# Optimization experiments

Measured on AMD Instinct MI355X. Metric: run time of the kernel, lower is better.

Reference implementation:

```python
import jax, jax.numpy as jnp
import numpy as np

OVERALL_W = (0.4, 0.4, 0.1, 0.1)


def nn_distance(pc1, pc2):
    # pc1: (B,N,3), pc2: (B,M,3) -> squared NN distance each way.
    # ||a-b||^2 = ||a||^2 + ||b||^2 - 2 a.b ; compute via batched GEMM.
    n1 = jnp.sum(pc1 * pc1, axis=-1)  # (B,N)
    n2 = jnp.sum(pc2 * pc2, axis=-1)  # (B,M)
    cross = jnp.einsum('bnd,bmd->bnm', pc1, pc2)  # (B,N,M)
    d = n1[:, :, None] + n2[:, None, :] - 2.0 * cross  # (B,N,M)
    dist1 = jnp.min(d, axis=2)  # (B,N)
    dist2 = jnp.min(d, axis=1)  # (B,M)
    return dist1, dist2


def setup_inputs() -> dict:
    key = jax.random.key(0)
    ks = jax.random.split(key, 7)
    bs, n_pts, num_hypo, cap_len = 16, 4096, 64, 77
    return {
        'shape_query': jax.random.normal(ks[0], (bs, n_pts, 3), dtype=jnp.float32),
        'logits': jax.random.normal(ks[1], (bs, num_hypo), dtype=jnp.float32),
        'pair_caption': jax.random.randint(ks[2], (bs, 2, cap_len), 0, 30000),
        'caption_embed': jax.random.randint(ks[3], (bs, 3, cap_len), 0, 30000),
        'sdf_pred': jax.random.normal(ks[4], (bs, 1, n_pts), dtype=jnp.float32),
        'prior': jax.random.normal(ks[5], (bs, 1024, 3), dtype=jnp.float32),
        'model': jax.random.normal(ks[6], (bs, 4096, 3), dtype=jnp.float32),
    }


def reference(shape_query, logits, pair_caption, caption_embed, sdf_pred, prior, model):
    log_prob = jax.nn.log_softmax(logits, axis=-1)
    pose_loss = -jnp.mean(log_prob[:, 0])
    reconstructed = jnp.concatenate([shape_query, prior], axis=1)  # (B, N+1024, 3)
    dist1, dist2 = nn_distance(reconstructed, model)
    shape_loss = jnp.mean(dist1) + jnp.mean(dist2)
    sdf_loss = shape_loss
    caption_loss = shape_loss
    loss = (OVERALL_W[0] * pose_loss + OVERALL_W[1] * shape_loss
            + OVERALL_W[2] * sdf_loss + OVERALL_W[3] * caption_loss)
    return (loss, pose_loss, shape_loss, sdf_loss, caption_loss)
```

## Files before the change

kernel.cpp:

```cpp
#include <hip/hip_runtime.h>
#include <math.h>

#define BATCH   16
#define NQ      4096
#define NPRIOR  1024
#define NREC    5120
#define NMODEL  4096
#define NHYP    64

#define NQD1    (BATCH*NREC)
#define NQD2    (BATCH*NMODEL)

#define TILE_COLS 512
#define P1_ROWBLKS (NREC/128)
#define P2_ROWBLKS (NMODEL/128)
#define P1_CHUNKS 2
#define P2_CHUNKS 2
#define P1_NTILES (NMODEL/TILE_COLS/P1_CHUNKS)
#define P2_NTILES (NREC/TILE_COLS/P2_CHUNKS)
#define P1_BLOCKS (BATCH*P1_ROWBLKS*P1_CHUNKS)
#define P2_BLOCKS (BATCH*P2_ROWBLKS*P2_CHUNKS)
#define GBLOCKS   (P1_BLOCKS + P2_BLOCKS)

#define WS_WORDS (P1_CHUNKS*NQD1 + P2_CHUNKS*NQD2 + 1)
#define WS_BYTES ((size_t)WS_WORDS*4)
#define RED_BLOCKS 128

typedef _Float16 half8  __attribute__((ext_vector_type(8)));
typedef float    f32x16 __attribute__((ext_vector_type(16)));

__device__ __forceinline__ float min3f(float a, float b, float c) {
    float d;
    asm("v_min3_f32 %0, %1, %2, %3" : "=v"(d) : "v"(a), "v"(b), "v"(c));
    return d;
}

__device__ __forceinline__ void packQ2(float x, float y, float z,
                                       half8& hi, half8& lo) {
    float n = fmaf(z, z, fmaf(y, y, x * x));
    float mx = -2.0f * x, my = -2.0f * y, mz = -2.0f * z;
    _Float16 xh = (_Float16)mx, yh = (_Float16)my, zh = (_Float16)mz;
    _Float16 nh = (_Float16)n;
    _Float16 xl = (_Float16)(mx - (float)xh);
    _Float16 yl = (_Float16)(my - (float)yh);
    _Float16 zl = (_Float16)(mz - (float)zh);
    _Float16 nl = (_Float16)(n - (float)nh);
    hi[0] = xh; hi[1] = yh; hi[2] = zh; hi[3] = nh;
    hi[4] = (_Float16)1.0f; hi[5] = xh; hi[6] = yh; hi[7] = zh;
    lo[0] = xl; lo[1] = yl; lo[2] = zl; lo[3] = nl;
    lo[4] = (_Float16)1.0f; lo[5] = (_Float16)0.0f;
    lo[6] = (_Float16)0.0f; lo[7] = (_Float16)0.0f;
}
__device__ __forceinline__ void packR2(float x, float y, float z,
                                       half8& hi, half8& lo) {
    float n = fmaf(z, z, fmaf(y, y, x * x));
    _Float16 xh = (_Float16)x, yh = (_Float16)y, zh = (_Float16)z;
    _Float16 nh = (_Float16)n;
    _Float16 xl = (_Float16)(x - (float)xh);
    _Float16 yl = (_Float16)(y - (float)yh);
    _Float16 zl = (_Float16)(z - (float)zh);
    _Float16 nl = (_Float16)(n - (float)nh);
    hi[0] = xh; hi[1] = yh; hi[2] = zh; hi[3] = (_Float16)1.0f;
    hi[4] = nh; hi[5] = xl; hi[6] = yl; hi[7] = zl;
    lo[0] = xh; lo[1] = yh; lo[2] = zh; lo[3] = (_Float16)1.0f;
    lo[4] = nl; lo[5] = (_Float16)0.0f;
    lo[6] = (_Float16)0.0f; lo[7] = (_Float16)0.0f;
}

__device__ __forceinline__ const float* rec_ptr(
    const float* __restrict__ shape_query, const float* __restrict__ prior,
    int b, int g) {
    return (g < NQ) ? shape_query + ((size_t)b * NQ + g) * 3
                    : prior + ((size_t)b * NPRIOR + (g - NQ)) * 3;
}

__global__ __launch_bounds__(256) void chamfer_hp(
    const float* __restrict__ shape_query,
    const float* __restrict__ prior,
    const float* __restrict__ model,
    float* __restrict__ ws, float* __restrict__ out) {
    __shared__ half8 Alds2[2 * 128];
    __shared__ half8 Blds2[2 * TILE_COLS];

    const int blk = blockIdx.x;
    if (blk == 0 && threadIdx.x == 0) {
        out[2] = 0.0f; out[3] = 0.0f;
        ((unsigned*)ws)[WS_WORDS - 1] = 0u;
    }

    const int t    = threadIdx.x;
    const int wave = t >> 6;
    const int lane = t & 63;
    const int l31  = lane & 31;
    const int kh   = lane >> 5;

    int b, rowbase, colbase0, ntiles;
    float* rowplane;
    const bool pass1 = (blk < P1_BLOCKS);
    if (pass1) {
        b = blk / (P1_ROWBLKS * P1_CHUNKS);
        int rem = blk % (P1_ROWBLKS * P1_CHUNKS);
        int rb = rem / P1_CHUNKS, ck = rem % P1_CHUNKS;
        rowbase = rb * 128;
        colbase0 = ck * (P1_NTILES * TILE_COLS);
        ntiles = P1_NTILES;
        rowplane = ws + (size_t)ck * NQD1 + b * NREC + rowbase;
    } else {
        int j = blk - P1_BLOCKS;
        b = j / (P2_ROWBLKS * P2_CHUNKS);
        int rem = j % (P2_ROWBLKS * P2_CHUNKS);
        int rb = rem / P2_CHUNKS, ck = rem % P2_CHUNKS;
        rowbase = rb * 128;
        colbase0 = ck * (P2_NTILES * TILE_COLS);
        ntiles = P2_NTILES;
        rowplane = ws + (size_t)P1_CHUNKS * NQD1 + (size_t)ck * NQD2
                   + b * NMODEL + rowbase;
    }

    if (t < 128) {
        const float* p = pass1
            ? rec_ptr(shape_query, prior, b, rowbase + t)
            : model + ((size_t)b * NMODEL + rowbase + t) * 3;
        half8 hi, lo;
        packQ2(p[0], p[1], p[2], hi, lo);
        Alds2[t] = hi; Alds2[128 + t] = lo;
    }

    {
        const float* p0 = pass1
            ? model + ((size_t)b * NMODEL + colbase0 + t) * 3
            : rec_ptr(shape_query, prior, b, colbase0 + t);
        const float* p1 = pass1
            ? model + ((size_t)b * NMODEL + colbase0 + 256 + t) * 3
            : rec_ptr(shape_query, prior, b, colbase0 + 256 + t);
        half8 hi, lo;
        packR2(p0[0], p0[1], p0[2], hi, lo);
        Blds2[t] = hi; Blds2[TILE_COLS + t] = lo;
        packR2(p1[0], p1[1], p1[2], hi, lo);
        Blds2[256 + t] = hi; Blds2[TILE_COLS + 256 + t] = lo;
    }

    float rmn[16];
#pragma unroll
    for (int r = 0; r < 16; ++r) rmn[r] = 3.0e38f;

    f32x16 cz;
#pragma unroll
    for (int i = 0; i < 16; ++i) cz[i] = 0.0f;

    const int boff = kh * TILE_COLS;

    __syncthreads();

    for (int tile = 0; tile < ntiles; ++tile) {
        float nx0, ny0, nz0, nx1, ny1, nz1;
        const bool more = (tile + 1 < ntiles);
        if (more) {
            const int cb = colbase0 + (tile + 1) * TILE_COLS;
            const float* p0 = pass1
                ? model + ((size_t)b * NMODEL + cb + t) * 3
                : rec_ptr(shape_query, prior, b, cb + t);
            const float* p1 = pass1
                ? model + ((size_t)b * NMODEL + cb + 256 + t) * 3
                : rec_ptr(shape_query, prior, b, cb + 256 + t);
            nx0 = p0[0]; ny0 = p0[1]; nz0 = p0[2];
            nx1 = p1[0]; ny1 = p1[1]; nz1 = p1[2];
        }

        half8 af = Alds2[kh * 128 + wave * 32 + l31];
        half8 bfa = Blds2[boff + l31];
        half8 bfb = Blds2[boff + 32 + l31];
#pragma unroll 2
        for (int it = 0; it < TILE_COLS / 64; ++it) {
            const int nxt = (it == TILE_COLS / 64 - 1) ? 0 : (it + 1) * 64;
            half8 bfa_n = Blds2[boff + nxt + l31];
            half8 bfb_n = Blds2[boff + nxt + 32 + l31];
            f32x16 da = __builtin_amdgcn_mfma_f32_32x32x16_f16(af, bfa, cz, 0, 0, 0);
            f32x16 db = __builtin_amdgcn_mfma_f32_32x32x16_f16(af, bfb, cz, 0, 0, 0);
#pragma unroll
            for (int r = 0; r < 16; ++r) rmn[r] = min3f(rmn[r], da[r], db[r]);
            bfa = bfa_n; bfb = bfb_n;
        }

        __syncthreads();
        if (more) {
            half8 hi, lo;
            packR2(nx0, ny0, nz0, hi, lo);
            Blds2[t] = hi; Blds2[TILE_COLS + t] = lo;
            packR2(nx1, ny1, nz1, hi, lo);
            Blds2[256 + t] = hi; Blds2[TILE_COLS + 256 + t] = lo;
            __syncthreads();
        }
    }

#pragma unroll
    for (int r = 0; r < 16; ++r) {
        float v = rmn[r];
        v = fminf(v, __shfl_xor(v, 1, 64));
        v = fminf(v, __shfl_xor(v, 2, 64));
        v = fminf(v, __shfl_xor(v, 4, 64));
        v = fminf(v, __shfl_xor(v, 8, 64));
        v = fminf(v, __shfl_xor(v, 16, 64));
        if (l31 == 0) {
            int row = wave * 32 + (r & 3) + 8 * (r >> 2) + 4 * kh;
            rowplane[row] = v;
        }
    }
}

__global__ __launch_bounds__(256) void reduce_finalize2(
    const float* __restrict__ ws, const float* __restrict__ logits,
    float* __restrict__ out, unsigned int* __restrict__ counter) {
    const float* p1 = ws;
    const float* p2 = ws + (size_t)P1_CHUNKS * NQD1;
    float s1 = 0.0f, s2 = 0.0f;
    const int tot = NQD1 + NQD2;
    for (int i = blockIdx.x * 256 + threadIdx.x; i < tot;
         i += RED_BLOCKS * 256) {
        if (i < NQD1) {
            s1 += fminf(p1[i], p1[NQD1 + i]);
        } else {
            int j = i - NQD1;
            s2 += fminf(p2[j], p2[NQD2 + j]);
        }
    }
#pragma unroll
    for (int off = 32; off > 0; off >>= 1) {
        s1 += __shfl_xor(s1, off, 64);
        s2 += __shfl_xor(s2, off, 64);
    }
    __shared__ float a1[4], a2[4];
    __shared__ int last;
    int w = threadIdx.x >> 6;
    if ((threadIdx.x & 63) == 0) { a1[w] = s1; a2[w] = s2; }
    __syncthreads();
    if (threadIdx.x == 0) {
        atomicAdd(&out[2], a1[0] + a1[1] + a1[2] + a1[3]);
        atomicAdd(&out[3], a2[0] + a2[1] + a2[2] + a2[3]);
        __threadfence();
        unsigned done = atomicAdd(counter, 1u);
        last = (done == RED_BLOCKS - 1) ? 1 : 0;
    }
    __syncthreads();
    if (last && threadIdx.x < 64) {
        const int lane = threadIdx.x;
        float pose_part = 0.0f;
        if (lane < BATCH) {
            const float* L = logits + lane * NHYP;
            float mx = L[0];
#pragma unroll 8
            for (int j = 1; j < NHYP; ++j) mx = fmaxf(mx, L[j]);
            float s = 0.0f;
#pragma unroll 8
            for (int j = 0; j < NHYP; ++j) s += expf(L[j] - mx);
            pose_part = L[0] - (mx + logf(s));
        }
#pragma unroll
        for (int off = 8; off > 0; off >>= 1)
            pose_part += __shfl_xor(pose_part, off, 64);
        if (lane == 0) {
            float sum1 = atomicAdd(&out[2], 0.0f);
            float sum2 = atomicAdd(&out[3], 0.0f);
            float shape_loss = sum1 / (float)NQD1 + sum2 / (float)NQD2;
            float pose_loss = -pose_part / (float)BATCH;
            out[0] = 0.4f * pose_loss + 0.6f * shape_loss;
            out[1] = pose_loss;
            out[2] = shape_loss;
            out[3] = shape_loss;
            out[4] = shape_loss;
        }
    }
}


__global__ void init_out(float* out) {
    if (threadIdx.x == 0) { out[2] = 0.0f; out[3] = 0.0f; }
}

__device__ __forceinline__ void scan_refs(const float* __restrict__ r, int cnt,
                                          float px, float py, float pz,
                                          float& minv) {
    for (int m = 0; m < cnt; m += 8) {
#pragma unroll
        for (int u = 0; u < 8; ++u) {
            float mx = r[(m + u) * 3 + 0];
            float my = r[(m + u) * 3 + 1];
            float mz = r[(m + u) * 3 + 2];
            float dx = px - mx, dy = py - my, dz = pz - mz;
            float d = fmaf(dz, dz, fmaf(dy, dy, dx * dx));
            minv = fminf(minv, d);
        }
    }
}

__global__ __launch_bounds__(64) void chamfer_sum(
    const float* __restrict__ qa, int na_, const float* __restrict__ qb, int nb_,
    const float* __restrict__ ra, int ma, const float* __restrict__ rb, int mb,
    float* __restrict__ accum) {
    const int b = blockIdx.y;
    const int n = blockIdx.x * 64 + threadIdx.x;
    float px, py, pz;
    if (n < na_) {
        const float* p = qa + ((size_t)b * na_ + n) * 3;
        px = p[0]; py = p[1]; pz = p[2];
    } else {
        const float* p = qb + ((size_t)b * nb_ + (n - na_)) * 3;
        px = p[0]; py = p[1]; pz = p[2];
    }
    float minv = 3.0e38f;
    scan_refs(ra + (size_t)b * ma * 3, ma, px, py, pz, minv);
    if (mb > 0) scan_refs(rb + (size_t)b * mb * 3, mb, px, py, pz, minv);
    float s = minv;
#pragma unroll
    for (int off = 32; off > 0; off >>= 1) s += __shfl_xor(s, off, 64);
    if (threadIdx.x == 0) atomicAdd(accum, s);
}

__global__ __launch_bounds__(64) void finalize_kernel(
    const float* __restrict__ logits, float* __restrict__ out) {
    const int lane = threadIdx.x;
    float pose_part = 0.0f;
    if (lane < BATCH) {
        const float* L = logits + lane * NHYP;
        float mx = L[0];
#pragma unroll 8
        for (int j = 1; j < NHYP; ++j) mx = fmaxf(mx, L[j]);
        float s = 0.0f;
#pragma unroll 8
        for (int j = 0; j < NHYP; ++j) s += expf(L[j] - mx);
        pose_part = L[0] - (mx + logf(s));
    }
#pragma unroll
    for (int off = 8; off > 0; off >>= 1) pose_part += __shfl_xor(pose_part, off, 64);
    if (lane == 0) {
        float shape_loss = out[2] / (float)NQD1 + out[3] / (float)NQD2;
        float pose_loss = -pose_part / (float)BATCH;
        out[0] = 0.4f * pose_loss + 0.6f * shape_loss;
        out[1] = pose_loss;
        out[2] = shape_loss;
        out[3] = shape_loss;
        out[4] = shape_loss;
    }
}

extern "C" void kernel_launch(void* const* d_in, const int* in_sizes, int n_in,
                              void* d_out, int out_size, void* d_ws, size_t ws_size,
                              hipStream_t stream) {
    const float* shape_query = (const float*)d_in[0];
    const float* logits      = (const float*)d_in[1];
    const float* prior       = (const float*)d_in[5];
    const float* model       = (const float*)d_in[6];
    float* out = (float*)d_out;

    if (ws_size >= WS_BYTES) {
        float* ws = (float*)d_ws;
        unsigned int* counter = (unsigned int*)ws + (WS_WORDS - 1);
        hipLaunchKernelGGL(chamfer_hp, dim3(GBLOCKS), dim3(256), 0, stream,
                           shape_query, prior, model, ws, out);
        hipLaunchKernelGGL(reduce_finalize2, dim3(RED_BLOCKS), dim3(256), 0,
                           stream, ws, logits, out, counter);
    } else {
        hipLaunchKernelGGL(init_out, dim3(1), dim3(64), 0, stream, out);
        hipLaunchKernelGGL(chamfer_sum,
                           dim3(NREC / 64, BATCH), dim3(64), 0, stream,
                           shape_query, NQ, prior, NPRIOR,
                           model, NMODEL, (const float*)nullptr, 0, out + 2);
        hipLaunchKernelGGL(chamfer_sum,
                           dim3(NMODEL / 64, BATCH), dim3(64), 0, stream,
                           model, NMODEL, (const float*)nullptr, 0,
                           shape_query, NQ, prior, NPRIOR, out + 3);
        hipLaunchKernelGGL(finalize_kernel, dim3(1), dim3(64), 0, stream,
                           logits, out);
    }
}
```

Baseline: 57.81 us.

## Split tile columns across waves so each wave covers all 128 rows

```diff
diff --git a/kernel.cpp b/kernel.cpp
--- a/kernel.cpp
+++ b/kernel.cpp
@@ -12,6 +12,7 @@
 #define NQD2    (BATCH*NMODEL)
 
 #define TILE_COLS 512
+#define WAVE_COLS 128
 #define P1_ROWBLKS (NREC/128)
 #define P2_ROWBLKS (NMODEL/128)
 #define P1_CHUNKS 2
@@ -81,6 +82,7 @@
     float* __restrict__ ws, float* __restrict__ out) {
     __shared__ half8 Alds2[2 * 128];
     __shared__ half8 Blds2[2 * TILE_COLS];
+    __shared__ float rowbuf[4 * 128];
 
     const int blk = blockIdx.x;
     if (blk == 0 && threadIdx.x == 0) {
@@ -140,17 +142,33 @@
         Blds2[256 + t] = hi; Blds2[TILE_COLS + 256 + t] = lo;
     }
 
-    float rmn[16];
-#pragma unroll
-    for (int r = 0; r < 16; ++r) rmn[r] = 3.0e38f;
+    float rmn0[16], rmn1[16], rmn2[16], rmn3[16];
+#pragma unroll
+    for (int r = 0; r < 16; ++r) {
+        rmn0[r] = 3.0e38f; rmn1[r] = 3.0e38f;
+        rmn2[r] = 3.0e38f; rmn3[r] = 3.0e38f;
+    }
 
     f32x16 cz;
 #pragma unroll
     for (int i = 0; i < 16; ++i) cz[i] = 0.0f;
 
-    const int boff = kh * TILE_COLS;
-
     __syncthreads();
+
+    half8 af0 = Alds2[kh * 128 + l31];
+    half8 af1 = Alds2[kh * 128 + 32 + l31];
+    half8 af2 = Alds2[kh * 128 + 64 + l31];
+    half8 af3 = Alds2[kh * 128 + 96 + l31];
+
+    const int bbase = kh * TILE_COLS + wave * WAVE_COLS;
+
+#define DOPAIR(AF, RM)                                                     \
+    {                                                                      \
+        f32x16 dA = __builtin_amdgcn_mfma_f32_32x32x16_f16(AF, bfx, cz, 0, 0, 0); \
+        f32x16 dB = __builtin_amdgcn_mfma_f32_32x32x16_f16(AF, bfy, cz, 0, 0, 0); \
+        _Pragma("unroll")                                                  \
+        for (int r = 0; r < 16; ++r) RM[r] = min3f(RM[r], dA[r], dB[r]);   \
+    }
 
     for (int tile = 0; tile < ntiles; ++tile) {
         float nx0, ny0, nz0, nx1, ny1, nz1;
@@ -167,19 +185,19 @@
             nx1 = p1[0]; ny1 = p1[1]; nz1 = p1[2];
         }
 
-        half8 af = Alds2[kh * 128 + wave * 32 + l31];
-        half8 bfa = Blds2[boff + l31];
-        half8 bfb = Blds2[boff + 32 + l31];
-#pragma unroll 2
-        for (int it = 0; it < TILE_COLS / 64; ++it) {
-            const int nxt = (it == TILE_COLS / 64 - 1) ? 0 : (it + 1) * 64;
-            half8 bfa_n = Blds2[boff + nxt + l31];
-            half8 bfb_n = Blds2[boff + nxt + 32 + l31];
-            f32x16 da = __builtin_amdgcn_mfma_f32_32x32x16_f16(af, bfa, cz, 0, 0, 0);
-            f32x16 db = __builtin_amdgcn_mfma_f32_32x32x16_f16(af, bfb, cz, 0, 0, 0);
-#pragma unroll
-            for (int r = 0; r < 16; ++r) rmn[r] = min3f(rmn[r], da[r], db[r]);
-            bfa = bfa_n; bfb = bfb_n;
+        {
+            half8 bfx = Blds2[bbase + l31];
+            half8 bfy = Blds2[bbase + 32 + l31];
+            DOPAIR(af0, rmn0)
+            DOPAIR(af1, rmn1)
+            DOPAIR(af2, rmn2)
+            DOPAIR(af3, rmn3)
+            bfx = Blds2[bbase + 64 + l31];
+            bfy = Blds2[bbase + 96 + l31];
+            DOPAIR(af0, rmn0)
+            DOPAIR(af1, rmn1)
+            DOPAIR(af2, rmn2)
+            DOPAIR(af3, rmn3)
         }
 
         __syncthreads();
@@ -192,19 +210,32 @@
             __syncthreads();
         }
     }
-
-#pragma unroll
-    for (int r = 0; r < 16; ++r) {
-        float v = rmn[r];
-        v = fminf(v, __shfl_xor(v, 1, 64));
-        v = fminf(v, __shfl_xor(v, 2, 64));
-        v = fminf(v, __shfl_xor(v, 4, 64));
-        v = fminf(v, __shfl_xor(v, 8, 64));
-        v = fminf(v, __shfl_xor(v, 16, 64));
-        if (l31 == 0) {
-            int row = wave * 32 + (r & 3) + 8 * (r >> 2) + 4 * kh;
-            rowplane[row] = v;
-        }
+#undef DOPAIR
+
+#define FLUSH(RM, A)                                                       \
+    _Pragma("unroll")                                                      \
+    for (int r = 0; r < 16; ++r) {                                         \
+        float v = RM[r];                                                   \
+        v = fminf(v, __shfl_xor(v, 1, 64));                                \
+        v = fminf(v, __shfl_xor(v, 2, 64));                                \
+        v = fminf(v, __shfl_xor(v, 4, 64));                                \
+        v = fminf(v, __shfl_xor(v, 8, 64));                                \
+        v = fminf(v, __shfl_xor(v, 16, 64));                               \
+        if (l31 == 0) {                                                    \
+            int row = (A) * 32 + (r & 3) + 8 * (r >> 2) + 4 * kh;          \
+            rowbuf[wave * 128 + row] = v;                                  \
+        }                                                                  \
+    }
+    FLUSH(rmn0, 0)
+    FLUSH(rmn1, 1)
+    FLUSH(rmn2, 2)
+    FLUSH(rmn3, 3)
+#undef FLUSH
+    __syncthreads();
+    if (t < 128) {
+        float v = fminf(fminf(rowbuf[t], rowbuf[128 + t]),
+                        fminf(rowbuf[256 + t], rowbuf[384 + t]));
+        rowplane[t] = v;
     }
 }
 
```

Measured after the change: 85.25 us. 47.5% more time.
